# Kernel optimization log

Measured on AMD Instinct MI355X. Metric: run time of the kernel, lower is better.

The kernel has to match this reference:

```python
import jax, jax.numpy as jnp
import numpy as np

EPS = 0.5          # entropy_epsilon
TAU = 0.5          # tau = 1 * entropy_epsilon
MAXITER = 10

NABLA_W = np.array([[[[0., 0., 0.], [0., -1., 0.], [0., 1., 0.]]],
                    [[[0., 0., 0.], [0., -1., 1.], [0., 0., 0.]]]], dtype=np.float32)  # (2,1,3,3)
DIV_W = np.array([[[[0., -1., 0.], [0., 1., 0.], [0., 0., 0.]],
                   [[0., 0., 0.], [-1., 1., 0.], [0., 0., 0.]]]], dtype=np.float32)    # (1,2,3,3)


def _conv(x, w):
    # x: (B,C,H,W), w: (O,I,3,3), padding=1 -> SAME
    return jax.lax.conv_general_dilated(
        x, w, window_strides=(1, 1), padding='SAME',
        dimension_numbers=('NCHW', 'OIHW', 'NCHW'))


def setup_inputs() -> dict:
    key = jax.random.key(0)
    k1, k2 = jax.random.split(key)
    B, H, W = 8, 1024, 1024
    o = jax.random.normal(k1, (B, 1, H, W), dtype=jnp.float32)
    vector_field = jax.random.normal(k2, (H, W, 2), dtype=jnp.float32)
    nabla_w = jnp.asarray(NABLA_W)
    div_w = jnp.asarray(DIV_W)
    return {"o": o, "vector_field": vector_field, "nabla_w": nabla_w, "div_w": div_w}


def reference(o, vector_field, nabla_w, div_w):
    o = o[:, 0]                      # (B,H,W)
    vf1 = vector_field[:, :, 1]      # (H,W)
    vf0 = vector_field[:, :, 0]      # (H,W)
    u = jax.nn.sigmoid(o / EPS)
    q = jnp.zeros_like(o)
    Tq = jnp.zeros_like(o)
    for _ in range(MAXITER):
        u_nabla = _conv(u[:, None], nabla_w)          # (B,2,H,W)
        q = q - TAU * (u_nabla[:, 0] * vf1 + u_nabla[:, 1] * vf0)
        q = jnp.maximum(q, 0.0)
        Tq = _conv(jnp.stack([vf1 * q, vf0 * q], axis=1), div_w)[:, 0]  # (B,H,W)
        u = jax.nn.sigmoid((o - Tq) / EPS)
    u1 = (o - Tq) / EPS
    return u1
```

## Files before the change

### kernel.cpp

```cpp
#include <hip/hip_runtime.h>
#include <math.h>

#define IMG_H 1024
#define IMG_W 1024
#define IMG_B 8
#define TPB 1024
#define RPB 32
#define BANDS (IMG_H / RPB)
#define NBLK (IMG_B * BANDS)

__device__ __forceinline__ float sig2(float x) {
    return 1.0f / (1.0f + __expf(-2.0f * x));
}
__device__ __forceinline__ int imax(int a, int b) { return a > b ? a : b; }
__device__ __forceinline__ int imin(int a, int b) { return a < b ? a : b; }

template<int D, bool READQ, bool FINAL>
__global__ __launch_bounds__(TPB, 8) void k_pipe(const float* __restrict__ qin,
                                                 const float* __restrict__ vf,
                                                 const float* __restrict__ o,
                                                 float* __restrict__ out) {
    __shared__ float sp[2][TPB + 1];
    __shared__ float su[D][2][TPB + 1];

    const int img = blockIdx.x / BANDS;
    const int r0  = (blockIdx.x % BANDS) * RPB;
    const int tid = threadIdx.x;
    const size_t ibase = (size_t)img * IMG_H * IMG_W;

    if (tid == 0) {
        sp[0][0] = 0.0f; sp[1][0] = 0.0f;
#pragma unroll
        for (int l = 0; l < D; ++l) { su[l][0][TPB] = 0.0f; su[l][1][TPB] = 0.0f; }
    }

    constexpr int HALO = FINAL ? 1 : 0;
    constexpr int NOH  = FINAL ? D + 1 : D;

    const int u0lo = imax(r0 - (D - 1) - HALO, 0);
    const int ylo  = READQ ? imax(r0 - D - HALO, 0) : u0lo;
    const int yend = r0 + RPB - 1 + D;
    const int yhi  = imin(yend, IMG_H - 1);

    float qc = 0.0f, qz = 0.0f;
    float oh[NOH];
    float v0h[D + 1], v1h[D + 1];
    float uY[D], uZ[D];
    float p1prev[D + 1];
    float qsave[D];
    float qvPrev = 0.0f;

#pragma unroll
    for (int l = 0; l < NOH; ++l) oh[l] = 0.0f;
#pragma unroll
    for (int l = 0; l <= D; ++l) { v0h[l] = 0.0f; v1h[l] = 0.0f; p1prev[l] = 0.0f; }
#pragma unroll
    for (int l = 0; l < D; ++l) { uY[l] = 0.0f; uZ[l] = 0.0f; qsave[l] = 0.0f; }

    const float* pQ = qin + ibase + (size_t)ylo * IMG_W + tid;
    const float* pO = o   + ibase + (size_t)ylo * IMG_W + tid;
    const float* pV = vf  + ((size_t)ylo * IMG_W + tid) * 2;

    for (int y = ylo; y <= yend; ++y) {
#pragma unroll
        for (int k = NOH - 1; k >= 1; --k) oh[k] = oh[k - 1];
#pragma unroll
        for (int k = D; k >= 1; --k) { v0h[k] = v0h[k - 1]; v1h[k] = v1h[k - 1]; }
        if constexpr (READQ) qz = qc;

        if (y <= yhi) {
            if constexpr (READQ) { qc = *pQ; pQ += IMG_W; }
            oh[0] = *pO; pO += IMG_W;
            float2 v2 = *(const float2*)pV; pV += 2 * IMG_W;
            v0h[0] = v2.x; v1h[0] = v2.y;
        } else {
            qc = 0.0f; oh[0] = 0.0f; v0h[0] = 0.0f; v1h[0] = 0.0f;
        }

        if constexpr (READQ) {
            float p0c = v0h[0] * qc;
            float p1c = v1h[0] * qc;
            sp[0][tid + 1] = p0c;
            __syncthreads();
            if (y >= u0lo) {
                float pm1 = sp[0][tid];
                float nu = (y <= IMG_H - 1)
                    ? sig2(oh[0] - (p1c - p1prev[0] + p0c - pm1)) : 0.0f;
                uZ[0] = uY[0]; uY[0] = nu;
                su[0][y & 1][tid] = nu;
            }
            p1prev[0] = p1c;
        } else {
            float nu = (y <= IMG_H - 1) ? sig2(oh[0]) : 0.0f;
            uZ[0] = uY[0]; uY[0] = nu;
            su[0][y & 1][tid] = nu;
        }

#pragma unroll
        for (int l = 1; l <= D; ++l) {
            const int t = y - l;
            const int qlo = imax(r0 - (D - l) - HALO, 0);
            const bool qvalid = (t >= qlo) && (t <= IMG_H - 1);
            float qbase = (l == 1) ? (READQ ? qz : 0.0f) : qsave[l - 1];
            if (l >= 2) qsave[l - 1] = qvPrev;
            float qv;
            if (qvalid) {
                const float uR = su[l - 1][t & 1][tid + 1];
                float gy = uY[l - 1] - uZ[l - 1];
                float gx = uR - uZ[l - 1];
                qv = fmaxf(qbase - 0.5f * (gy * v1h[l] + gx * v0h[l]), 0.0f);
            } else {
                qv = 0.0f;
            }

            if (l < D) {
                float p0p = v0h[l] * qv;
                float p1p = v1h[l] * qv;
                sp[l & 1][tid + 1] = p0p;
                __syncthreads();
                const int ulo = imax(r0 - (D - 1 - l) - HALO, 0);
                if (t >= ulo) {
                    float pm1 = sp[l & 1][tid];
                    float nu = (t <= IMG_H - 1)
                        ? sig2(oh[l] - (p1p - p1prev[l] + p0p - pm1)) : 0.0f;
                    uZ[l] = uY[l]; uY[l] = nu;
                    su[l][t & 1][tid] = nu;
                }
                p1prev[l] = p1p;
            } else {
                if constexpr (FINAL) {
                    float p0p = v0h[D] * qv;
                    float p1p = v1h[D] * qv;
                    sp[D & 1][tid + 1] = p0p;
                    __syncthreads();
                    if (t >= r0 && t < r0 + RPB) {
                        float pm1 = sp[D & 1][tid];
                        float Tq = p1p - p1prev[D] + p0p - pm1;
                        out[ibase + (size_t)t * IMG_W + tid] = 2.0f * (oh[D] - Tq);
                    }
                    p1prev[D] = p1p;
                } else {
                    if (t >= r0 && t < r0 + RPB)
                        out[ibase + (size_t)t * IMG_W + tid] = qv;
                }
            }
            qvPrev = qv;
        }
    }
}

extern "C" void kernel_launch(void* const* d_in, const int* in_sizes, int n_in,
                              void* d_out, int out_size, void* d_ws, size_t ws_size,
                              hipStream_t stream) {
    const float* o  = (const float*)d_in[0];
    const float* vf = (const float*)d_in[1];
    float* qA = (float*)d_ws;

    k_pipe<5, false, false><<<NBLK, TPB, 0, stream>>>(o, vf, o, qA);
    k_pipe<5, true,  true ><<<NBLK, TPB, 0, stream>>>(qA, vf, o, (float*)d_out);
}
```

Before: 258.2 us.

## Split image columns into two halves with halo to shrink blocks

Each band block now covers half the image width plus a 6-column halo on each side, using 576 threads instead of 1024. Block count doubles. Out-of-range columns and rows are handled by setting o to -1e30 so the sigmoid yields zero, which replaces the explicit row bounds checks. The intent is cheaper __syncthreads across fewer waves and better occupancy and scheduling, at the cost of about 12% redundant halo computation.

```diff
diff --git a/kernel.cpp b/kernel.cpp
--- a/kernel.cpp
+++ b/kernel.cpp
@@ -4,10 +4,13 @@
 #define IMG_H 1024
 #define IMG_W 1024
 #define IMG_B 8
-#define TPB 1024
+#define TPB 576
 #define RPB 32
 #define BANDS (IMG_H / RPB)
-#define NBLK (IMG_B * BANDS)
+#define XSPL 2
+#define XOUT 512
+#define XHALO 6
+#define NBLK (IMG_B * BANDS * XSPL)
 
 __device__ __forceinline__ float sig2(float x) {
     return 1.0f / (1.0f + __expf(-2.0f * x));
@@ -16,16 +19,23 @@
 __device__ __forceinline__ int imin(int a, int b) { return a < b ? a : b; }
 
 template<int D, bool READQ, bool FINAL>
-__global__ __launch_bounds__(TPB, 8) void k_pipe(const float* __restrict__ qin,
+__global__ __launch_bounds__(TPB, 5) void k_pipe(const float* __restrict__ qin,
                                                  const float* __restrict__ vf,
                                                  const float* __restrict__ o,
                                                  float* __restrict__ out) {
     __shared__ float sp[2][TPB + 1];
     __shared__ float su[D][2][TPB + 1];
 
-    const int img = blockIdx.x / BANDS;
-    const int r0  = (blockIdx.x % BANDS) * RPB;
-    const int tid = threadIdx.x;
+    const int b    = blockIdx.x;
+    const int xh   = b & (XSPL - 1);
+    const int band = (b >> 1) & (BANDS - 1);
+    const int img  = b >> 6;
+    const int r0   = band * RPB;
+    const int tid  = threadIdx.x;
+    const int x    = xh * XOUT - XHALO + tid;
+    const bool ok  = ((unsigned)x < (unsigned)IMG_W);
+    const int  xc  = imin(imax(x, 0), IMG_W - 1);
+    const bool wr  = (tid >= XHALO) && (tid < XHALO + XOUT);
     const size_t ibase = (size_t)img * IMG_H * IMG_W;
 
     if (tid == 0) {
@@ -51,15 +61,15 @@
     float qvPrev = 0.0f;
 
 #pragma unroll
-    for (int l = 0; l < NOH; ++l) oh[l] = 0.0f;
+    for (int l = 0; l < NOH; ++l) oh[l] = -1e30f;
 #pragma unroll
     for (int l = 0; l <= D; ++l) { v0h[l] = 0.0f; v1h[l] = 0.0f; p1prev[l] = 0.0f; }
 #pragma unroll
     for (int l = 0; l < D; ++l) { uY[l] = 0.0f; uZ[l] = 0.0f; qsave[l] = 0.0f; }
 
-    const float* pQ = qin + ibase + (size_t)ylo * IMG_W + tid;
-    const float* pO = o   + ibase + (size_t)ylo * IMG_W + tid;
-    const float* pV = vf  + ((size_t)ylo * IMG_W + tid) * 2;
+    const float* pQ = qin + ibase + (size_t)ylo * IMG_W + xc;
+    const float* pO = o   + ibase + (size_t)ylo * IMG_W + xc;
+    const float* pV = vf  + ((size_t)ylo * IMG_W + xc) * 2;
 
     for (int y = ylo; y <= yend; ++y) {
 #pragma unroll
@@ -70,11 +80,13 @@
 
         if (y <= yhi) {
             if constexpr (READQ) { qc = *pQ; pQ += IMG_W; }
-            oh[0] = *pO; pO += IMG_W;
+            float ov = *pO; pO += IMG_W;
+            oh[0] = ok ? ov : -1e30f;
             float2 v2 = *(const float2*)pV; pV += 2 * IMG_W;
-            v0h[0] = v2.x; v1h[0] = v2.y;
+            v0h[0] = ok ? v2.x : 0.0f;
+            v1h[0] = ok ? v2.y : 0.0f;
         } else {
-            qc = 0.0f; oh[0] = 0.0f; v0h[0] = 0.0f; v1h[0] = 0.0f;
+            qc = 0.0f; oh[0] = -1e30f; v0h[0] = 0.0f; v1h[0] = 0.0f;
         }
 
         if constexpr (READQ) {
@@ -84,14 +96,13 @@
             __syncthreads();
             if (y >= u0lo) {
                 float pm1 = sp[0][tid];
-                float nu = (y <= IMG_H - 1)
-                    ? sig2(oh[0] - (p1c - p1prev[0] + p0c - pm1)) : 0.0f;
+                float nu = sig2(oh[0] - (p1c - p1prev[0] + p0c - pm1));
                 uZ[0] = uY[0]; uY[0] = nu;
                 su[0][y & 1][tid] = nu;
             }
             p1prev[0] = p1c;
         } else {
-            float nu = (y <= IMG_H - 1) ? sig2(oh[0]) : 0.0f;
+            float nu = sig2(oh[0]);
             uZ[0] = uY[0]; uY[0] = nu;
             su[0][y & 1][tid] = nu;
         }
@@ -121,8 +132,7 @@
                 const int ulo = imax(r0 - (D - 1 - l) - HALO, 0);
                 if (t >= ulo) {
                     float pm1 = sp[l & 1][tid];
-                    float nu = (t <= IMG_H - 1)
-                        ? sig2(oh[l] - (p1p - p1prev[l] + p0p - pm1)) : 0.0f;
+                    float nu = sig2(oh[l] - (p1p - p1prev[l] + p0p - pm1));
                     uZ[l] = uY[l]; uY[l] = nu;
                     su[l][t & 1][tid] = nu;
                 }
@@ -136,12 +146,13 @@
                     if (t >= r0 && t < r0 + RPB) {
                         float pm1 = sp[D & 1][tid];
                         float Tq = p1p - p1prev[D] + p0p - pm1;
-                        out[ibase + (size_t)t * IMG_W + tid] = 2.0f * (oh[D] - Tq);
+                        if (wr)
+                            out[ibase + (size_t)t * IMG_W + x] = 2.0f * (oh[D] - Tq);
                     }
                     p1prev[D] = p1p;
                 } else {
-                    if (t >= r0 && t < r0 + RPB)
-                        out[ibase + (size_t)t * IMG_W + tid] = qv;
+                    if (t >= r0 && t < r0 + RPB && wr)
+                        out[ibase + (size_t)t * IMG_W + x] = qv;
                 }
             }
             qvPrev = qv;
```

Result: no change. 259.1 us (+0.4%).
